# Optimization experiments

Hardware: AMD Instinct MI355X
Metric: run time of the kernel (lower is better)

## Reference

```python
import jax, jax.numpy as jnp
import numpy as np

M = 100_000   # output rows of neighborhood matrix
N = 100_000   # nodes
D = 64        # feature dim (in_channels)
OUT = 64      # out_channels
NNZ = 1_600_000
NEG_SLOPE = 0.2


def setup_inputs() -> dict:
    key = jax.random.key(0)
    k1, k2, k3, k4, k5 = jax.random.split(key, 5)
    # ensure every row has at least one neighbor (torch min init is +inf otherwise)
    rows = jnp.concatenate([jnp.arange(M, dtype=jnp.int32),
                            jax.random.randint(k1, (NNZ - M,), 0, M, dtype=jnp.int32)])
    cols = jax.random.randint(k2, (NNZ,), 0, N, dtype=jnp.int32)
    vals = jnp.ones((NNZ,), jnp.float32)
    node_features = jax.random.normal(k3, (N, D), jnp.float32)
    W = jax.random.normal(k4, (OUT, 12 * D), jnp.float32) / jnp.sqrt(12.0 * D)
    b = jax.random.normal(k5, (OUT,), jnp.float32) * 0.01
    return {"rows": rows, "cols": cols, "vals": vals,
            "node_features": node_features, "W": W, "b": b}


def reference(rows, cols, vals, node_features, W, b):
    gathered = node_features[cols]                      # [nnz, D]
    deg = jax.ops.segment_sum(vals, rows, num_segments=M)[:, None]  # [M,1]
    valid = deg > 0
    safe_deg = jnp.where(valid, deg, 1.0)

    # mean = spmm(A, X) / deg on valid rows (torch leaves invalid rows as raw sum = 0)
    sums = jax.ops.segment_sum(vals[:, None] * gathered, rows, num_segments=M)
    mean = jnp.where(valid, sums / safe_deg, sums)

    # torch max starts from zeros -> clamps at 0 from below; empty rows stay 0
    maxf = jnp.zeros((M, D), node_features.dtype).at[rows].max(gathered)
    # torch min starts from +inf; all rows covered by construction
    minf = jnp.full((M, D), jnp.inf, node_features.dtype).at[rows].min(gathered)

    sq = jax.ops.segment_sum(vals[:, None] * gathered**2, rows, num_segments=M)
    sq = jnp.where(valid, sq / safe_deg, sq)
    std = jnp.sqrt(jnp.clip(sq - mean**2, 0.0))

    logd = jnp.log10(deg + 2.0)                          # [M,1]
    delta = jnp.mean(logd)
    s = logd / delta

    # per aggregator: identity, amplification (*s), attenuation (/s)
    feats = [t for a in (mean, maxf, minf, std) for t in (a, a * s, a / s)]
    X = jnp.concatenate(feats, axis=1)                   # [M, 12*D]
    out = X @ W.T + b
    return jnp.where(out >= 0, out, NEG_SLOPE * out)
```

## Files before the change

### kernel.cpp

```cpp
#include <hip/hip_runtime.h>
#include <cstdint>

#define M_ROWS   100000
#define N_NODES  100000
#define NNZ_E    1600000
#define K_DIM    768
#define NCHUNK   24
#define NEG_SLOPE 0.2f
#define NBUK     391
#define BCAP     5120
#define EPB      4096

using f32x4 = __attribute__((ext_vector_type(4))) float;
using f16x8 = __attribute__((ext_vector_type(8))) _Float16;
using f16x4 = __attribute__((ext_vector_type(4))) _Float16;

#define OFF_CNT    0u
#define OFF_RS     401408u
#define OFF_PART   802816u
#define OFF_DELTA  804864u
#define OFF_GCUR   805120u
#define OFF_BINCSR 807168u
#define OFF_WB     8814848u
#define OFF_NFH    8913152u
#define WS_NEEDED  21713152u

__global__ void k_wb(const float* __restrict__ W, _Float16* __restrict__ Wb) {
  int idx = blockIdx.x * blockDim.x + threadIdx.x;
  if (idx < NCHUNK * 4 * 64 * 8) {
    int i  = idx & 7;
    int l  = (idx >> 3) & 63;
    int n  = (idx >> 9) & 3;
    int kc = idx >> 11;
    int k  = kc * 32 + ((l >> 4) << 3) + i;
    int o  = n * 16 + (l & 15);
    Wb[idx] = (_Float16)W[o * K_DIM + k];
  }
}

__global__ void k_nf(const float* __restrict__ nf, _Float16* __restrict__ nfh,
                     int* __restrict__ gcur) {
  const int gid = blockIdx.x * 256 + threadIdx.x;
  if (gid < NBUK) gcur[gid] = gid * BCAP;
  const int i = gid * 4;
  if (i < N_NODES * 64) {
    const f32x4 v = *reinterpret_cast<const f32x4*>(nf + i);
    f16x4 h;
    #pragma unroll
    for (int j = 0; j < 4; ++j) h[j] = (_Float16)v[j];
    *reinterpret_cast<f16x4*>(nfh + i) = h;
  }
}

__global__ void k_seed(int* __restrict__ gcur) {
  int b = blockIdx.x * blockDim.x + threadIdx.x;
  if (b < NBUK) gcur[b] = b * BCAP;
}

__global__ __launch_bounds__(256) void k_bin(const int* __restrict__ rows,
                                             const int* __restrict__ cols,
                                             int* __restrict__ gcur,
                                             int* __restrict__ binArr) {
  __shared__ int hist[NBUK];
  __shared__ int base_s[NBUK];
  const int t  = threadIdx.x;
  const int e0 = blockIdx.x * EPB;
  for (int b = t; b < NBUK; b += 256) hist[b] = 0;
  __syncthreads();
  #pragma unroll
  for (int i = 0; i < EPB / 256; ++i) {
    const int e = e0 + i * 256 + t;
    if (e < NNZ_E) atomicAdd(&hist[rows[e] >> 8], 1);
  }
  __syncthreads();
  for (int b = t; b < NBUK; b += 256) {
    const int h = hist[b];
    base_s[b] = h ? atomicAdd(&gcur[b], h) : 0;
    hist[b] = 0;
  }
  __syncthreads();
  #pragma unroll
  for (int i = 0; i < EPB / 256; ++i) {
    const int e = e0 + i * 256 + t;
    if (e < NNZ_E) {
      const int r = rows[e], c = cols[e], b = r >> 8;
      const int p = atomicAdd(&hist[b], 1);
      const int slot = base_s[b] + p;
      if (slot < (b + 1) * BCAP)
        binArr[slot] = ((r & 255) << 24) | c;
    }
  }
}

__global__ __launch_bounds__(256) void k_sortbucket(int* __restrict__ bincsr,
                                                    const int* __restrict__ gcur,
                                                    int* __restrict__ cnt,
                                                    int* __restrict__ row_start,
                                                    float* __restrict__ partial) {
  __shared__ int se[BCAP];
  __shared__ int hist[256];
  __shared__ int curs[256];
  __shared__ int sd[256];
  __shared__ float wsum[4];
  const int b = blockIdx.x, t = threadIdx.x;
  const int s0  = b * BCAP;
  const int len = min(gcur[b] - s0, BCAP);
  for (int i = t; i < len; i += 256) se[i] = bincsr[s0 + i];
  hist[t] = 0;
  __syncthreads();
  for (int i = t; i < len; i += 256)
    atomicAdd(&hist[((unsigned)se[i]) >> 24], 1);
  __syncthreads();
  const int h = hist[t];
  const int r = (b << 8) + t;
  sd[t] = h;
  __syncthreads();
  #pragma unroll
  for (int off = 1; off < 256; off <<= 1) {
    int add = (t >= off) ? sd[t - off] : 0;
    __syncthreads();
    sd[t] += add;
    __syncthreads();
  }
  const int excl = sd[t] - h;
  curs[t] = excl;
  if (r < M_ROWS) {
    cnt[r] = h;
    row_start[r] = s0 + excl;
  }
  float ls = (r < M_ROWS) ? log10f((float)h + 2.0f) : 0.f;
  #pragma unroll
  for (int off = 32; off > 0; off >>= 1) ls += __shfl_xor(ls, off);
  if ((t & 63) == 0) wsum[t >> 6] = ls;
  __syncthreads();
  if (t == 0) partial[b] = wsum[0] + wsum[1] + wsum[2] + wsum[3];
  for (int i = t; i < len; i += 256) {
    const int e  = se[i];
    const int rl = (int)(((unsigned)e) >> 24);
    const int p  = atomicAdd(&curs[rl], 1);
    bincsr[s0 + p] = (e & 0x00FFFFFF) << 7;
  }
}

__global__ void k_delta(const float* __restrict__ partial, float* __restrict__ delta) {
  __shared__ float sd[256];
  const int t = threadIdx.x;
  float s = 0.f;
  for (int i = t; i < NBUK; i += 256) s += partial[i];
  sd[t] = s;
  __syncthreads();
  for (int off = 128; off > 0; off >>= 1) {
    if (t < off) sd[t] += sd[t + off];
    __syncthreads();
  }
  if (t == 0) delta[0] = sd[0] / (float)M_ROWS;
}

template <bool F16NF>
__global__ __launch_bounds__(256) void k_main(
    const float* __restrict__ nf32, const _Float16* __restrict__ nfh,
    const int* __restrict__ csr, const int* __restrict__ rs,
    const int* __restrict__ cnt, const float* __restrict__ delta_p,
    const _Float16* __restrict__ Wb, const float* __restrict__ bias,
    float* __restrict__ out)
{
  __shared__ _Float16 xs[32][264];
  __shared__ float s_s[32];

  const int tid  = threadIdx.x;
  const int w    = tid >> 6;
  const int lane = tid & 63;
  const int g    = lane >> 4;
  const int q    = lane & 15;
  const int h    = (lane >> 3) & 1;
  const int d    = lane & 7;
  const int r0   = blockIdx.x * 32;
  const float delta = delta_p[0];
  const int d16  = d * 16;

  auto ld16 = [&](int off) -> f16x8 {
    if constexpr (F16NF) {
      return *reinterpret_cast<const f16x8*>((const char*)nfh + off + d16);
    } else {
      const char* p = (const char*)nf32 + (size_t)off * 2 + d * 32;
      const f32x4 a = *reinterpret_cast<const f32x4*>(p);
      const f32x4 c = *reinterpret_cast<const f32x4*>(p + 16);
      f16x8 x;
      #pragma unroll
      for (int j = 0; j < 4; ++j) { x[j] = (_Float16)a[j]; x[4 + j] = (_Float16)c[j]; }
      return x;
    }
  };

  auto xor8 = [&](f16x8 v) -> f16x8 {
    union { f16x8 hh; int ii[4]; } u;
    u.hh = v;
    #pragma unroll
    for (int k = 0; k < 4; ++k) u.ii[k] = __shfl_xor(u.ii[k], 8);
    return u.hh;
  };

  #pragma unroll
  for (int pass = 0; pass < 2; ++pass) {
    const int rl  = w * 8 + pass * 4 + g;
    const int r   = r0 + rl;
    const int js  = rs[r];
    const int len = cnt[r];
    const int full8 = len & ~7;
    const int tailn = len - full8;
    int mfull = full8, mtail = tailn;
    mfull = max(mfull, __shfl_xor(mfull, 16));
    mfull = max(mfull, __shfl_xor(mfull, 32));
    mtail = max(mtail, __shfl_xor(mtail, 16));
    mtail = max(mtail, __shfl_xor(mtail, 32));

    f16x8 hsum = {}; f16x8 hsq = {}; f16x8 hmx = {};
    f16x8 hmn = {(_Float16)INFINITY, (_Float16)INFINITY, (_Float16)INFINITY,
                 (_Float16)INFINITY, (_Float16)INFINITY, (_Float16)INFINITY,
                 (_Float16)INFINITY, (_Float16)INFINITY};

    const int jb = js + h;

    for (int t = 0; t < mfull; t += 8) {
      if (t < full8) {
        const int i0 = csr[jb + t + 0];
        const int i1 = csr[jb + t + 2];
        const int i2 = csr[jb + t + 4];
        const int i3 = csr[jb + t + 6];
        const f16x8 x0 = ld16(i0), x1 = ld16(i1), x2 = ld16(i2), x3 = ld16(i3);
        hmx = __builtin_elementwise_max(hmx, x0);
        hmn = __builtin_elementwise_min(hmn, x0);
        hsum += x0; hsq += x0 * x0;
        hmx = __builtin_elementwise_max(hmx, x1);
        hmn = __builtin_elementwise_min(hmn, x1);
        hsum += x1; hsq += x1 * x1;
        hmx = __builtin_elementwise_max(hmx, x2);
        hmn = __builtin_elementwise_min(hmn, x2);
        hsum += x2; hsq += x2 * x2;
        hmx = __builtin_elementwise_max(hmx, x3);
        hmn = __builtin_elementwise_min(hmn, x3);
        hsum += x3; hsq += x3 * x3;
      }
    }

    if (mtail > 0) {
      const int last = js + len - 1;
      const int e0 = full8 + 0 + h, e1 = full8 + 2 + h;
      const int e2 = full8 + 4 + h, e3 = full8 + 6 + h;
      const int i0 = csr[min(jb + full8 + 0, last)];
      const int i1 = csr[min(jb + full8 + 2, last)];
      const int i2 = csr[min(jb + full8 + 4, last)];
      const int i3 = csr[min(jb + full8 + 6, last)];
      const f16x8 x0 = ld16(i0), x1 = ld16(i1), x2 = ld16(i2), x3 = ld16(i3);
      const f16x8 z = {};
      const f16x8 m0 = (e0 < len) ? x0 : z;
      const f16x8 m1 = (e1 < len) ? x1 : z;
      const f16x8 m2 = (e2 < len) ? x2 : z;
      const f16x8 m3 = (e3 < len) ? x3 : z;
      hmx = __builtin_elementwise_max(hmx, x0);
      hmn = __builtin_elementwise_min(hmn, x0);
      hsum += m0; hsq += m0 * x0;
      hmx = __builtin_elementwise_max(hmx, x1);
      hmn = __builtin_elementwise_min(hmn, x1);
      hsum += m1; hsq += m1 * x1;
      hmx = __builtin_elementwise_max(hmx, x2);
      hmn = __builtin_elementwise_min(hmn, x2);
      hsum += m2; hsq += m2 * x2;
      hmx = __builtin_elementwise_max(hmx, x3);
      hmn = __builtin_elementwise_min(hmn, x3);
      hsum += m3; hsq += m3 * x3;
    }

    hsum += xor8(hsum);
    hsq  += xor8(hsq);
    hmx = __builtin_elementwise_max(hmx, xor8(hmx));
    hmn = __builtin_elementwise_min(hmn, xor8(hmn));

    const float dg  = (float)len;
    const float inv = 1.0f / fmaxf(dg, 1.0f);
    f16x8 hmean, hstd;
    #pragma unroll
    for (int i = 0; i < 8; ++i) {
      const float mean = (float)hsum[i] * inv;
      const float sqm  = (float)hsq[i] * inv;
      const float var  = fmaxf(sqm - mean * mean, 0.f);
      hmean[i] = (_Float16)mean;
      hstd[i]  = (_Float16)sqrtf(var);
    }
    if (h == 0) {
      *reinterpret_cast<f16x8*>(&xs[rl][0 * 64 + d * 8]) = hmean;
      *reinterpret_cast<f16x8*>(&xs[rl][1 * 64 + d * 8]) = hmx;
      *reinterpret_cast<f16x8*>(&xs[rl][2 * 64 + d * 8]) = hmn;
      *reinterpret_cast<f16x8*>(&xs[rl][3 * 64 + d * 8]) = hstd;
      if (q == 0) s_s[rl] = log10f(dg + 2.0f) / delta;
    }
  }
  __syncthreads();

  f32x4 acc0 = {0.f, 0.f, 0.f, 0.f}, acc1 = {0.f, 0.f, 0.f, 0.f};
  const int khi = lane >> 4;
  const float sA = s_s[q];
  const float sB = s_s[16 + q];
  const f16x8 sA8  = (f16x8)(_Float16)sA;
  const f16x8 isA8 = (f16x8)(_Float16)(1.0f / sA);
  const f16x8 sB8  = (f16x8)(_Float16)sB;
  const f16x8 isB8 = (f16x8)(_Float16)(1.0f / sB);

  #pragma unroll
  for (int kc = 0; kc < NCHUNK; ++kc) {
    const int kb = kc >> 1;
    const int a  = kb / 3;
    const int tt = kb - 3 * a;
    const int off = a * 64 + ((kc & 1) << 5) + (khi << 3);
    f16x8 a0 = *reinterpret_cast<const f16x8*>(&xs[q][off]);
    f16x8 a1 = *reinterpret_cast<const f16x8*>(&xs[16 + q][off]);
    if (tt == 1) { a0 = a0 * sA8;  a1 = a1 * sB8; }
    if (tt == 2) { a0 = a0 * isA8; a1 = a1 * isB8; }
    const f16x8 bf = *reinterpret_cast<const f16x8*>(Wb + ((size_t)(kc * 4 + w) * 64 + lane) * 8);
    acc0 = __builtin_amdgcn_mfma_f32_16x16x32_f16(a0, bf, acc0, 0, 0, 0);
    acc1 = __builtin_amdgcn_mfma_f32_16x16x32_f16(a1, bf, acc1, 0, 0, 0);
  }

  const int col = w * 16 + q;
  const float bv = bias[col];
  #pragma unroll
  for (int i = 0; i < 4; ++i) {
    const int rr = khi * 4 + i;
    float v = acc0[i] + bv;
    v = (v >= 0.f) ? v : NEG_SLOPE * v;
    out[(size_t)(r0 + rr) * 64 + col] = v;
    float u = acc1[i] + bv;
    u = (u >= 0.f) ? u : NEG_SLOPE * u;
    out[(size_t)(r0 + 16 + rr) * 64 + col] = u;
  }
}

extern "C" void kernel_launch(void* const* d_in, const int* in_sizes, int n_in,
                              void* d_out, int out_size, void* d_ws, size_t ws_size,
                              hipStream_t stream) {
  const int*   rows = (const int*)d_in[0];
  const int*   cols = (const int*)d_in[1];
  const float* nf   = (const float*)d_in[3];
  const float* W    = (const float*)d_in[4];
  const float* bias = (const float*)d_in[5];
  float* out = (float*)d_out;

  char* ws = (char*)d_ws;
  int*      cnt       = (int*)(ws + OFF_CNT);
  int*      row_start = (int*)(ws + OFF_RS);
  float*    partial   = (float*)(ws + OFF_PART);
  float*    delta     = (float*)(ws + OFF_DELTA);
  int*      gcur      = (int*)(ws + OFF_GCUR);
  int*      bincsr    = (int*)(ws + OFF_BINCSR);
  _Float16* Wb        = (_Float16*)(ws + OFF_WB);
  _Float16* nfh       = (_Float16*)(ws + OFF_NFH);

  const bool f16path = (ws_size >= WS_NEEDED);

  k_wb<<<192, 256, 0, stream>>>(W, Wb);
  if (f16path) k_nf<<<6250, 256, 0, stream>>>(nf, nfh, gcur);
  else         k_seed<<<2, 256, 0, stream>>>(gcur);
  k_bin<<<(NNZ_E + EPB - 1) / EPB, 256, 0, stream>>>(rows, cols, gcur, bincsr);
  k_sortbucket<<<NBUK, 256, 0, stream>>>(bincsr, gcur, cnt, row_start, partial);
  k_delta<<<1, 256, 0, stream>>>(partial, delta);
  if (f16path)
    k_main<true><<<3125, 256, 0, stream>>>(nf, nfh, bincsr, row_start, cnt, delta, Wb, bias, out);
  else
    k_main<false><<<3125, 256, 0, stream>>>(nf, nfh, bincsr, row_start, cnt, delta, Wb, bias, out);
}
```

Before: 103.6 us.

## Fuse W and feature conversion kernels, double bin chunk, persist main tiles

Merges the weight fp16 conversion into the node-feature conversion kernel, which removes one launch. Doubles the edges handled per binning block and drops the unroll pragmas there. Makes the main kernel loop over row tiles with a grid of half the tile count, so each block handles about two tiles, with an extra barrier between tiles. Fewer launches and fewer blocks cut setup overhead, but the grid may now be too small to hide gather latency.

After: 133.3 us. 28.7% more time.

```diff
diff --git a/kernel.cpp b/kernel.cpp
--- a/kernel.cpp
+++ b/kernel.cpp
@@ -9,7 +9,11 @@
 #define NEG_SLOPE 0.2f
 #define NBUK     391
 #define BCAP     5120
-#define EPB      4096
+#define EPB      8192
+#define NTILE    3125
+#define GMAIN    1563
+#define WB_ELEMS (NCHUNK * 4 * 64 * 8)
+#define NFWB_BLOCKS ((N_NODES * 16 + WB_ELEMS + 255) / 256)
 
 using f32x4 = __attribute__((ext_vector_type(4))) float;
 using f16x8 = __attribute__((ext_vector_type(8))) _Float16;
@@ -27,7 +31,7 @@
 
 __global__ void k_wb(const float* __restrict__ W, _Float16* __restrict__ Wb) {
   int idx = blockIdx.x * blockDim.x + threadIdx.x;
-  if (idx < NCHUNK * 4 * 64 * 8) {
+  if (idx < WB_ELEMS) {
     int i  = idx & 7;
     int l  = (idx >> 3) & 63;
     int n  = (idx >> 9) & 3;
@@ -38,17 +42,31 @@
   }
 }
 
-__global__ void k_nf(const float* __restrict__ nf, _Float16* __restrict__ nfh,
-                     int* __restrict__ gcur) {
+__global__ __launch_bounds__(256) void k_nfwb(const float* __restrict__ nf,
+                                              _Float16* __restrict__ nfh,
+                                              const float* __restrict__ W,
+                                              _Float16* __restrict__ Wb,
+                                              int* __restrict__ gcur) {
   const int gid = blockIdx.x * 256 + threadIdx.x;
   if (gid < NBUK) gcur[gid] = gid * BCAP;
-  const int i = gid * 4;
-  if (i < N_NODES * 64) {
+  if (gid < N_NODES * 16) {
+    const int i = gid * 4;
     const f32x4 v = *reinterpret_cast<const f32x4*>(nf + i);
     f16x4 h;
     #pragma unroll
     for (int j = 0; j < 4; ++j) h[j] = (_Float16)v[j];
     *reinterpret_cast<f16x4*>(nfh + i) = h;
+  } else {
+    const int idx = gid - N_NODES * 16;
+    if (idx < WB_ELEMS) {
+      const int i  = idx & 7;
+      const int l  = (idx >> 3) & 63;
+      const int n  = (idx >> 9) & 3;
+      const int kc = idx >> 11;
+      const int k  = kc * 32 + ((l >> 4) << 3) + i;
+      const int o  = n * 16 + (l & 15);
+      Wb[idx] = (_Float16)W[o * K_DIM + k];
+    }
   }
 }
 
@@ -67,7 +85,6 @@
   const int e0 = blockIdx.x * EPB;
   for (int b = t; b < NBUK; b += 256) hist[b] = 0;
   __syncthreads();
-  #pragma unroll
   for (int i = 0; i < EPB / 256; ++i) {
     const int e = e0 + i * 256 + t;
     if (e < NNZ_E) atomicAdd(&hist[rows[e] >> 8], 1);
@@ -79,7 +96,6 @@
     hist[b] = 0;
   }
   __syncthreads();
-  #pragma unroll
   for (int i = 0; i < EPB / 256; ++i) {
     const int e = e0 + i * 256 + t;
     if (e < NNZ_E) {
@@ -174,7 +190,6 @@
   const int q    = lane & 15;
   const int h    = (lane >> 3) & 1;
   const int d    = lane & 7;
-  const int r0   = blockIdx.x * 32;
   const float delta = delta_p[0];
   const int d16  = d * 16;
 
@@ -200,138 +215,143 @@
     return u.hh;
   };
 
-  #pragma unroll
-  for (int pass = 0; pass < 2; ++pass) {
-    const int rl  = w * 8 + pass * 4 + g;
-    const int r   = r0 + rl;
-    const int js  = rs[r];
-    const int len = cnt[r];
-    const int full8 = len & ~7;
-    const int tailn = len - full8;
-    int mfull = full8, mtail = tailn;
-    mfull = max(mfull, __shfl_xor(mfull, 16));
-    mfull = max(mfull, __shfl_xor(mfull, 32));
-    mtail = max(mtail, __shfl_xor(mtail, 16));
-    mtail = max(mtail, __shfl_xor(mtail, 32));
-
-    f16x8 hsum = {}; f16x8 hsq = {}; f16x8 hmx = {};
-    f16x8 hmn = {(_Float16)INFINITY, (_Float16)INFINITY, (_Float16)INFINITY,
-                 (_Float16)INFINITY, (_Float16)INFINITY, (_Float16)INFINITY,
-                 (_Float16)INFINITY, (_Float16)INFINITY};
-
-    const int jb = js + h;
-
-    for (int t = 0; t < mfull; t += 8) {
-      if (t < full8) {
-        const int i0 = csr[jb + t + 0];
-        const int i1 = csr[jb + t + 2];
-        const int i2 = csr[jb + t + 4];
-        const int i3 = csr[jb + t + 6];
+  for (int tile = blockIdx.x; tile < NTILE; tile += GMAIN) {
+    const int r0 = tile * 32;
+
+    #pragma unroll
+    for (int pass = 0; pass < 2; ++pass) {
+      const int rl  = w * 8 + pass * 4 + g;
+      const int r   = r0 + rl;
+      const int js  = rs[r];
+      const int len = cnt[r];
+      const int full8 = len & ~7;
+      const int tailn = len - full8;
+      int mfull = full8, mtail = tailn;
+      mfull = max(mfull, __shfl_xor(mfull, 16));
+      mfull = max(mfull, __shfl_xor(mfull, 32));
+      mtail = max(mtail, __shfl_xor(mtail, 16));
+      mtail = max(mtail, __shfl_xor(mtail, 32));
+
+      f16x8 hsum = {}; f16x8 hsq = {}; f16x8 hmx = {};
+      f16x8 hmn = {(_Float16)INFINITY, (_Float16)INFINITY, (_Float16)INFINITY,
+                   (_Float16)INFINITY, (_Float16)INFINITY, (_Float16)INFINITY,
+                   (_Float16)INFINITY, (_Float16)INFINITY};
+
+      const int jb = js + h;
+
+      for (int t = 0; t < mfull; t += 8) {
+        if (t < full8) {
+          const int i0 = csr[jb + t + 0];
+          const int i1 = csr[jb + t + 2];
+          const int i2 = csr[jb + t + 4];
+          const int i3 = csr[jb + t + 6];
+          const f16x8 x0 = ld16(i0), x1 = ld16(i1), x2 = ld16(i2), x3 = ld16(i3);
+          hmx = __builtin_elementwise_max(hmx, x0);
+          hmn = __builtin_elementwise_min(hmn, x0);
+          hsum += x0; hsq += x0 * x0;
+          hmx = __builtin_elementwise_max(hmx, x1);
+          hmn = __builtin_elementwise_min(hmn, x1);
+          hsum += x1; hsq += x1 * x1;
+          hmx = __builtin_elementwise_max(hmx, x2);
+          hmn = __builtin_elementwise_min(hmn, x2);
+          hsum += x2; hsq += x2 * x2;
+          hmx = __builtin_elementwise_max(hmx, x3);
+          hmn = __builtin_elementwise_min(hmn, x3);
+          hsum += x3; hsq += x3 * x3;
+        }
+      }
+
+      if (mtail > 0) {
+        const int last = js + len - 1;
+        const int e0 = full8 + 0 + h, e1 = full8 + 2 + h;
+        const int e2 = full8 + 4 + h, e3 = full8 + 6 + h;
+        const int i0 = csr[min(jb + full8 + 0, last)];
+        const int i1 = csr[min(jb + full8 + 2, last)];
+        const int i2 = csr[min(jb + full8 + 4, last)];
+        const int i3 = csr[min(jb + full8 + 6, last)];
         const f16x8 x0 = ld16(i0), x1 = ld16(i1), x2 = ld16(i2), x3 = ld16(i3);
+        const f16x8 z = {};
+        const f16x8 m0 = (e0 < len) ? x0 : z;
+        const f16x8 m1 = (e1 < len) ? x1 : z;
+        const f16x8 m2 = (e2 < len) ? x2 : z;
+        const f16x8 m3 = (e3 < len) ? x3 : z;
         hmx = __builtin_elementwise_max(hmx, x0);
         hmn = __builtin_elementwise_min(hmn, x0);
-        hsum += x0; hsq += x0 * x0;
+        hsum += m0; hsq += m0 * x0;
         hmx = __builtin_elementwise_max(hmx, x1);
         hmn = __builtin_elementwise_min(hmn, x1);
-        hsum += x1; hsq += x1 * x1;
+        hsum += m1; hsq += m1 * x1;
         hmx = __builtin_elementwise_max(hmx, x2);
         hmn = __builtin_elementwise_min(hmn, x2);
-        hsum += x2; hsq += x2 * x2;
+        hsum += m2; hsq += m2 * x2;
         hmx = __builtin_elementwise_max(hmx, x3);
         hmn = __builtin_elementwise_min(hmn, x3);
-        hsum += x3; hsq += x3 * x3;
+        hsum += m3; hsq += m3 * x3;
       }
-    }
-
-    if (mtail > 0) {
-      const int last = js + len - 1;
-      const int e0 = full8 + 0 + h, e1 = full8 + 2 + h;
-      const int e2 = full8 + 4 + h, e3 = full8 + 6 + h;
-      const int i0 = csr[min(jb + full8 + 0, last)];
-      const int i1 = csr[min(jb + full8 + 2, last)];
-      const int i2 = csr[min(jb + full8 + 4, last)];
-      const int i3 = csr[min(jb + full8 + 6, last)];
-      const f16x8 x0 = ld16(i0), x1 = ld16(i1), x2 = ld16(i2), x3 = ld16(i3);
-      const f16x8 z = {};
-      const f16x8 m0 = (e0 < len) ? x0 : z;
-      const f16x8 m1 = (e1 < len) ? x1 : z;
-      const f16x8 m2 = (e2 < len) ? x2 : z;
-      const f16x8 m3 = (e3 < len) ? x3 : z;
-      hmx = __builtin_elementwise_max(hmx, x0);
-      hmn = __builtin_elementwise_min(hmn, x0);
-      hsum += m0; hsq += m0 * x0;
-      hmx = __builtin_elementwise_max(hmx, x1);
-      hmn = __builtin_elementwise_min(hmn, x1);
-      hsum += m1; hsq += m1 * x1;
-      hmx = __builtin_elementwise_max(hmx, x2);
-      hmn = __builtin_elementwise_min(hmn, x2);
-      hsum += m2; hsq += m2 * x2;
-      hmx = __builtin_elementwise_max(hmx, x3);
-      hmn = __builtin_elementwise_min(hmn, x3);
-      hsum += m3; hsq += m3 * x3;
-    }
-
-    hsum += xor8(hsum);
-    hsq  += xor8(hsq);
-    hmx = __builtin_elementwise_max(hmx, xor8(hmx));
-    hmn = __builtin_elementwise_min(hmn, xor8(hmn));
-
-    const float dg  = (float)len;
-    const float inv = 1.0f / fmaxf(dg, 1.0f);
-    f16x8 hmean, hstd;
-    #pragma unroll
-    for (int i = 0; i < 8; ++i) {
-      const float mean = (float)hsum[i] * inv;
-      const float sqm  = (float)hsq[i] * inv;
-      const float var  = fmaxf(sqm - mean * mean, 0.f);
-      hmean[i] = (_Float16)mean;
-      hstd[i]  = (_Float16)sqrtf(var);
-    }
-    if (h == 0) {
-      *reinterpret_cast<f16x8*>(&xs[rl][0 * 64 + d * 8]) = hmean;
-      *reinterpret_cast<f16x8*>(&xs[rl][1 * 64 + d * 8]) = hmx;
-      *reinterpret_cast<f16x8*>(&xs[rl][2 * 64 + d * 8]) = hmn;
-      *reinterpret_cast<f16x8*>(&xs[rl][3 * 64 + d * 8]) = hstd;
-      if (q == 0) s_s[rl] = log10f(dg + 2.0f) / delta;
-    }
-  }
-  __syncthreads();
-
-  f32x4 acc0 = {0.f, 0.f, 0.f, 0.f}, acc1 = {0.f, 0.f, 0.f, 0.f};
-  const int khi = lane >> 4;
-  const float sA = s_s[q];
-  const float sB = s_s[16 + q];
-  const f16x8 sA8  = (f16x8)(_Float16)sA;
-  const f16x8 isA8 = (f16x8)(_Float16)(1.0f / sA);
-  const f16x8 sB8  = (f16x8)(_Float16)sB;
-  const f16x8 isB8 = (f16x8)(_Float16)(1.0f / sB);
-
-  #pragma unroll
-  for (int kc = 0; kc < NCHUNK; ++kc) {
-    const int kb = kc >> 1;
-    const int a  = kb / 3;
-    const int tt = kb - 3 * a;
-    const int off = a * 64 + ((kc & 1) << 5) + (khi << 3);
-    f16x8 a0 = *reinterpret_cast<const f16x8*>(&xs[q][off]);
-    f16x8 a1 = *reinterpret_cast<const f16x8*>(&xs[16 + q][off]);
-    if (tt == 1) { a0 = a0 * sA8;  a1 = a1 * sB8; }
-    if (tt == 2) { a0 = a0 * isA8; a1 = a1 * isB8; }
-    const f16x8 bf = *reinterpret_cast<const f16x8*>(Wb + ((size_t)(kc * 4 + w) * 64 + lane) * 8);
-    acc0 = __builtin_amdgcn_mfma_f32_16x16x32_f16(a0, bf, acc0, 0, 0, 0);
-    acc1 = __builtin_amdgcn_mfma_f32_16x16x32_f16(a1, bf, acc1, 0, 0, 0);
-  }
-
-  const int col = w * 16 + q;
-  const float bv = bias[col];
-  #pragma unroll
-  for (int i = 0; i < 4; ++i) {
-    const int rr = khi * 4 + i;
-    float v = acc0[i] + bv;
-    v = (v >= 0.f) ? v : NEG_SLOPE * v;
-    out[(size_t)(r0 + rr) * 64 + col] = v;
-    float u = acc1[i] + bv;
-    u = (u >= 0.f) ? u : NEG_SLOPE * u;
-    out[(size_t)(r0 + 16 + rr) * 64 + col] = u;
+
+      hsum += xor8(hsum);
+      hsq  += xor8(hsq);
+      hmx = __builtin_elementwise_max(hmx, xor8(hmx));
+      hmn = __builtin_elementwise_min(hmn, xor8(hmn));
+
+      const float dg  = (float)len;
+      const float inv = 1.0f / fmaxf(dg, 1.0f);
+      f16x8 hmean, hstd;
+      #pragma unroll
+      for (int i = 0; i < 8; ++i) {
+        const float mean = (float)hsum[i] * inv;
+        const float sqm  = (float)hsq[i] * inv;
+        const float var  = fmaxf(sqm - mean * mean, 0.f);
+        hmean[i] = (_Float16)mean;
+        hstd[i]  = (_Float16)sqrtf(var);
+      }
+      if (h == 0) {
+        *reinterpret_cast<f16x8*>(&xs[rl][0 * 64 + d * 8]) = hmean;
+        *reinterpret_cast<f16x8*>(&xs[rl][1 * 64 + d * 8]) = hmx;
+        *reinterpret_cast<f16x8*>(&xs[rl][2 * 64 + d * 8]) = hmn;
+        *reinterpret_cast<f16x8*>(&xs[rl][3 * 64 + d * 8]) = hstd;
+        if (q == 0) s_s[rl] = log10f(dg + 2.0f) / delta;
+      }
+    }
+    __syncthreads();
+
+    f32x4 acc0 = {0.f, 0.f, 0.f, 0.f}, acc1 = {0.f, 0.f, 0.f, 0.f};
+    const int khi = lane >> 4;
+    const float sA = s_s[q];
+    const float sB = s_s[16 + q];
+    const f16x8 sA8  = (f16x8)(_Float16)sA;
+    const f16x8 isA8 = (f16x8)(_Float16)(1.0f / sA);
+    const f16x8 sB8  = (f16x8)(_Float16)sB;
+    const f16x8 isB8 = (f16x8)(_Float16)(1.0f / sB);
+
+    #pragma unroll
+    for (int kc = 0; kc < NCHUNK; ++kc) {
+      const int kb = kc >> 1;
+      const int a  = kb / 3;
+      const int tt = kb - 3 * a;
+      const int off = a * 64 + ((kc & 1) << 5) + (khi << 3);
+      f16x8 a0 = *reinterpret_cast<const f16x8*>(&xs[q][off]);
+      f16x8 a1 = *reinterpret_cast<const f16x8*>(&xs[16 + q][off]);
+      if (tt == 1) { a0 = a0 * sA8;  a1 = a1 * sB8; }
+      if (tt == 2) { a0 = a0 * isA8; a1 = a1 * isB8; }
+      const f16x8 bf = *reinterpret_cast<const f16x8*>(Wb + ((size_t)(kc * 4 + w) * 64 + lane) * 8);
+      acc0 = __builtin_amdgcn_mfma_f32_16x16x32_f16(a0, bf, acc0, 0, 0, 0);
+      acc1 = __builtin_amdgcn_mfma_f32_16x16x32_f16(a1, bf, acc1, 0, 0, 0);
+    }
+
+    const int col = w * 16 + q;
+    const float bv = bias[col];
+    #pragma unroll
+    for (int i = 0; i < 4; ++i) {
+      const int rr = khi * 4 + i;
+      float v = acc0[i] + bv;
+      v = (v >= 0.f) ? v : NEG_SLOPE * v;
+      out[(size_t)(r0 + rr) * 64 + col] = v;
+      float u = acc1[i] + bv;
+      u = (u >= 0.f) ? u : NEG_SLOPE * u;
+      out[(size_t)(r0 + 16 + rr) * 64 + col] = u;
+    }
+    __syncthreads();
   }
 }
 
@@ -357,14 +377,17 @@
 
   const bool f16path = (ws_size >= WS_NEEDED);
 
-  k_wb<<<192, 256, 0, stream>>>(W, Wb);
-  if (f16path) k_nf<<<6250, 256, 0, stream>>>(nf, nfh, gcur);
-  else         k_seed<<<2, 256, 0, stream>>>(gcur);
+  if (f16path) {
+    k_nfwb<<<NFWB_BLOCKS, 256, 0, stream>>>(nf, nfh, W, Wb, gcur);
+  } else {
+    k_wb<<<192, 256, 0, stream>>>(W, Wb);
+    k_seed<<<2, 256, 0, stream>>>(gcur);
+  }
   k_bin<<<(NNZ_E + EPB - 1) / EPB, 256, 0, stream>>>(rows, cols, gcur, bincsr);
   k_sortbucket<<<NBUK, 256, 0, stream>>>(bincsr, gcur, cnt, row_start, partial);
   k_delta<<<1, 256, 0, stream>>>(partial, delta);
   if (f16path)
-    k_main<true><<<3125, 256, 0, stream>>>(nf, nfh, bincsr, row_start, cnt, delta, Wb, bias, out);
+    k_main<true><<<GMAIN, 256, 0, stream>>>(nf, nfh, bincsr, row_start, cnt, delta, Wb, bias, out);
   else
-    k_main<false><<<3125, 256, 0, stream>>>(nf, nfh, bincsr, row_start, cnt, delta, Wb, bias, out);
-}
+    k_main<false><<<GMAIN, 256, 0, stream>>>(nf, nfh, bincsr, row_start, cnt, delta, Wb, bias, out);
+}
```
